# Optimization experiments

Hardware: AMD Instinct MI355X
Metric: run time of the kernel (lower is better)

The kernel has to match this reference:

```python
import jax, jax.numpy as jnp
import numpy as np

HQ, HKV, D, NE = 8, 2, 48, 384   # query heads, kv heads, head_size, n_embd
GROUP = HQ // HKV                # query heads per kv head (repeat_interleave factor)
ROPE_BASE = 10000
NEG_INF = -1e30


def rope_cache(T, head_dim):
    # matches build_rope_cache: inv_freq over even indices, angles = pos * inv_freq
    inv_freq = 1.0 / (ROPE_BASE ** (jnp.arange(0, head_dim, 2, dtype=jnp.float32) / head_dim))
    pos = jnp.arange(T, dtype=jnp.float32)
    ang = pos[:, None] * inv_freq[None, :]          # [T, D/2]
    return jnp.cos(ang), jnp.sin(ang)


def apply_rope(x, cos, sin):
    # interleaved (even/odd) rotation, re-interleaved via stack+reshape
    xe = x[..., 0::2]
    xo = x[..., 1::2]
    re = xe * cos - xo * sin
    ro = xe * sin + xo * cos
    return jnp.stack((re, ro), axis=-1).reshape(x.shape)


def setup_inputs() -> dict:
    key = jax.random.key(0)
    ks = jax.random.split(key, 6)
    B, T = 8, 2048
    s = lambda n: 1.0 / np.sqrt(n)
    return {
        "x":  jax.random.normal(ks[0], (B, T, NE), jnp.float32),
        "wq": jax.random.normal(ks[1], (NE, HQ * D), jnp.float32) * s(NE),
        "wk": jax.random.normal(ks[2], (NE, HKV * D), jnp.float32) * s(NE),
        "wv": jax.random.normal(ks[3], (NE, HKV * D), jnp.float32) * s(NE),
        "wo": jax.random.normal(ks[4], (NE, NE), jnp.float32) * s(NE),
        "bo": jnp.zeros((NE,), jnp.float32),
    }


def reference(x, wq, wk, wv, wo, bo):
    B, T, _ = x.shape
    # QKV projections (weights stored [in, out]); [B, H, T, D]
    q = (x @ wq).reshape(B, T, HQ, D).transpose(0, 2, 1, 3)
    k = (x @ wk).reshape(B, T, HKV, D).transpose(0, 2, 1, 3)
    v = (x @ wv).reshape(B, T, HKV, D).transpose(0, 2, 1, 3)

    cos, sin = rope_cache(T, D)                      # [T, D/2]
    cos = cos[None, None]                            # [1,1,T,D/2]
    sin = sin[None, None]
    q = apply_rope(q, cos, sin)
    k = apply_rope(k, cos, sin)

    # GQA: group query heads per kv head (math-identical to repeat_interleave on k/v)
    qg = q.reshape(B, HKV, GROUP, T, D)
    scale = 1.0 / np.sqrt(D)
    scores = jnp.einsum('bhgtd,bhsd->bhgts', qg, k) * scale   # [B,HKV,G,T,T]
    causal = jnp.tril(jnp.ones((T, T), dtype=bool))
    scores = jnp.where(causal, scores, NEG_INF)
    attn = jax.nn.softmax(scores, axis=-1)
    out = jnp.einsum('bhgts,bhsd->bhgtd', attn, v)            # [B,HKV,G,T,D]
    out = out.reshape(B, HQ, T, D).transpose(0, 2, 1, 3).reshape(B, T, NE)
    # output projection (eval mode: dropout is identity)
    return out @ wo + bo
```

## Files before the change

kernel.cpp:

```cpp
#include <hip/hip_runtime.h>
#include <math.h>

#define B_   8
#define T_   2048
#define NE_  384
#define HQ_  8
#define HKV_ 2
#define D_   48
#define DH_  24

typedef __attribute__((ext_vector_type(8))) short bf16x8;
typedef __attribute__((ext_vector_type(4))) short bf16x4;
typedef __attribute__((ext_vector_type(4))) float f32x4;

static __device__ __forceinline__ short f2bf(float f) {
    union { float f; unsigned u; } v; v.f = f;
    unsigned r = (v.u + 0x7fffu + ((v.u >> 16) & 1u)) >> 16;
    return (short)r;
}

static __device__ __forceinline__ float exp2_fast(float x) {
    float r;
    asm("v_exp_f32 %0, %1" : "=v"(r) : "v"(x));
    return r;
}
static __device__ __forceinline__ unsigned cvt_pk_bf16(float lo, float hi) {
    unsigned r;
    asm("v_cvt_pk_bf16_f32 %0, %1, %2" : "=v"(r) : "v"(lo), "v"(hi));
    return r;
}
static __device__ __forceinline__ float max3f(float a, float b, float c) {
    float r;
    asm("v_max3_f32 %0, %1, %2, %3" : "=v"(r) : "v"(a), "v"(b), "v"(c));
    return r;
}
static __device__ __forceinline__ void gld16(const void* g, void* l) {
    __builtin_amdgcn_global_load_lds(
        (const __attribute__((address_space(1))) unsigned int*)g,
        (__attribute__((address_space(3))) unsigned int*)l,
        16, 0, 0);
}

__global__ __launch_bounds__(256) void prep_kernel(
    const float* __restrict__ x, const float* __restrict__ wq,
    const float* __restrict__ wk, const float* __restrict__ wv,
    const float* __restrict__ wo,
    short* __restrict__ xb, short* __restrict__ wt, short* __restrict__ wot,
    float* __restrict__ ct, float* __restrict__ st)
{
    const int bid = blockIdx.x, tid = threadIdx.x;
    if (bid < 6144) {
        int i = bid * 256 + tid;
        float4 v = ((const float4*)x)[i];
        bf16x4 o = { f2bf(v.x), f2bf(v.y), f2bf(v.z), f2bf(v.w) };
        *(bf16x4*)&xb[(size_t)i * 4] = o;
    } else if (bid < 7008) {
        int e = (bid - 6144) * 256 + tid;
        int n = e / 384, k = e - n * 384;
        float s = (n < 384) ? wq[(size_t)k * 384 + n]
                : (n < 480) ? wk[(size_t)k * 96 + (n - 384)]
                            : wv[(size_t)k * 96 + (n - 480)];
        wt[e] = f2bf(s);
    } else if (bid < 7584) {
        int e = (bid - 7008) * 256 + tid;
        int n = e / 384, k = e - n * 384;
        wot[e] = f2bf(wo[(size_t)k * 384 + n]);
    } else {
        int i = (bid - 7584) * 256 + tid;
        int t = i / DH_, j = i - t * DH_;
        double inv = pow(10000.0, -(double)(2 * j) / (double)D_);
        double ang = (double)t * inv;
        ct[i] = (float)cos(ang);
        st[i] = (float)sin(ang);
    }
}

#define GP 40
__global__ __launch_bounds__(256) void qkv_gemm_kernel(
    const short* __restrict__ xb, const short* __restrict__ wt,
    const float* __restrict__ ct, const float* __restrict__ st,
    short* __restrict__ qb, short* __restrict__ kb, short* __restrict__ vtb)
{
    const int tid = threadIdx.x;
    const int n0 = blockIdx.x * 64;
    const int m0 = blockIdx.y * 128;
    __shared__ short As[128 * GP];
    __shared__ short Bs[64 * GP];
    const int lane = tid & 63, w = tid >> 6;
    const int c = lane & 15, u = lane >> 4;
    const int mo = (w & 1) * 64, no = (w >> 1) * 32;
    f32x4 acc[4][2] = {};

    for (int kt = 0; kt < 384; kt += 32) {
        __syncthreads();
#pragma unroll
        for (int p = 0; p < 2; ++p) {
            int f = tid + p * 256;
            int row = f >> 2, j = f & 3;
            bf16x8 v = *(const bf16x8*)&xb[(size_t)(m0 + row) * 384 + kt + j * 8];
            *(bf16x8*)&As[row * GP + j * 8] = v;
        }
        {
            int row = tid >> 2, j = tid & 3;
            bf16x8 v = *(const bf16x8*)&wt[(size_t)(n0 + row) * 384 + kt + j * 8];
            *(bf16x8*)&Bs[row * GP + j * 8] = v;
        }
        __syncthreads();
        bf16x8 af[4], bfr[2];
#pragma unroll
        for (int i = 0; i < 4; ++i) af[i] = *(bf16x8*)&As[(mo + 16 * i + c) * GP + 8 * u];
#pragma unroll
        for (int j = 0; j < 2; ++j) bfr[j] = *(bf16x8*)&Bs[(no + 16 * j + c) * GP + 8 * u];
#pragma unroll
        for (int i = 0; i < 4; ++i)
#pragma unroll
            for (int j = 0; j < 2; ++j)
                acc[i][j] = __builtin_amdgcn_mfma_f32_16x16x32_bf16(af[i], bfr[j], acc[i][j], 0, 0, 0);
    }

    const float qscale = 0.14433756729740643f * 1.4426950408889634f;
#pragma unroll
    for (int i = 0; i < 4; ++i) {
#pragma unroll
        for (int j = 0; j < 2; ++j) {
            int n = n0 + no + 16 * j + c;
            int mb = m0 + mo + 16 * i + 4 * u;
            int b = mb >> 11;
            int t0 = mb & 2047;
            if (n < 480) {
                int nn = (n < 384) ? n : n - 384;
                int h = nn / 48, d = nn - h * 48;
                int fi = d >> 1;
                float sgn = (d & 1) ? 1.0f : -1.0f;
                float scl = (n < 384) ? qscale : 1.0f;
                short* dst = (n < 384) ? qb : kb;
                size_t base = (n < 384)
                    ? ((size_t)(b * HQ_ + h) * T_ + t0) * 64 + d
                    : ((size_t)(b * HKV_ + h) * T_ + t0) * 64 + d;
#pragma unroll
                for (int r = 0; r < 4; ++r) {
                    float val = acc[i][j][r];
                    float part = __shfl_xor(val, 1);
                    float cs = ct[(t0 + r) * DH_ + fi], sn = st[(t0 + r) * DH_ + fi];
                    dst[base + (size_t)r * 64] = f2bf((val * cs + sgn * part * sn) * scl);
                }
            } else {
                int nn = n - 480;
                int h = nn / 48, d = nn - h * 48;
                ushort4 pk;
                pk.x = (unsigned short)f2bf(acc[i][j][0]);
                pk.y = (unsigned short)f2bf(acc[i][j][1]);
                pk.z = (unsigned short)f2bf(acc[i][j][2]);
                pk.w = (unsigned short)f2bf(acc[i][j][3]);
                *(ushort4*)&vtb[((size_t)(b * HKV_ + h) * D_ + d) * T_ + t0] = pk;
            }
        }
    }
}

__global__ __launch_bounds__(256, 2) void attn_kernel(
    const short* __restrict__ qb, const short* __restrict__ kb,
    const short* __restrict__ vtb, short* __restrict__ aob)
{
    __shared__ __align__(16) short lds_s[14336];
    const int tid = threadIdx.x;
    const int x  = blockIdx.x;
    const int hk = blockIdx.y >> 1;
    const int gp = blockIdx.y & 1;
    const int b  = blockIdx.z;
    const int lane = tid & 63;
    const int w = tid >> 6;
    const int c = lane & 15;
    const int u = lane >> 4;

    const char* kg = (const char*)kb  + (size_t)(b * HKV_ + hk) * T_ * 128;
    const char* vg = (const char*)vtb + (size_t)(b * HKV_ + hk) * D_ * T_ * 2;

    const int swz  = (lane ^ ((lane >> 3) & 7)) << 4;
    const int vrow = lane >> 3;
    const int voff = swz & 127;

    const int mk  = (c & 7) << 4;
    const int okl = (u * 16) ^ mk;
    const int okh = (64 | (u * 16)) ^ mk;

    auto stage = [&](int bsel, int jt) {
        char* dst = (char*)lds_s + bsel * 14336;
        const char* kt = kg + (size_t)jt * 8192;
        gld16(kt + (2 * w) * 1024 + swz,     dst + (2 * w) * 1024);
        gld16(kt + (2 * w + 1) * 1024 + swz, dst + (2 * w + 1) * 1024);
        if (w < 3) {
            const char* vt = vg + (size_t)jt * 128;
            gld16(vt + (size_t)(16 * w + vrow) * 4096 + voff,
                  dst + 8192 + (2 * w) * 1024);
            gld16(vt + (size_t)(16 * w + 8 + vrow) * 4096 + voff,
                  dst + 8192 + (2 * w + 1) * 1024);
        }
    };

#pragma unroll 1
    for (int ph = 0; ph < 2; ++ph) {
        const int qt = ph ? x : 31 - x;
        bf16x8 qf0[2], qf1[2];
#pragma unroll
        for (int g = 0; g < 2; ++g) {
            int h = hk * 4 + gp * 2 + g;
            const short* qp = qb + ((size_t)(b * HQ_ + h) * T_ + qt * 64 + 16 * w + c) * 64;
            qf0[g] = *(const bf16x8*)(qp + 8 * u);
            qf1[g] = *(const bf16x8*)(qp + 32 + 8 * u);
        }
        float m_s[2] = { -1e30f, -1e30f };
        float l_s[2] = { 0.f, 0.f };
        f32x4 o[2][3] = {};

        int cur = 0;
        stage(0, 0);
        __syncthreads();

#pragma unroll 1
        for (int jt = 0; jt <= qt; ++jt) {
            if (jt < qt) stage(cur ^ 1, jt + 1);

            const bool diag = (jt == qt);
            const int mtmax = diag ? (w + 1) : 4;
            const char* kbuf = (const char*)lds_s + cur * 14336;
            const char* vbuf = kbuf + 8192;

            bf16x8 klo[4], khi[4];
            bf16x4 vf[3][4];
#pragma unroll
            for (int mt = 0; mt < 4; ++mt) {
                if (mt < mtmax) {
                    klo[mt] = *(const bf16x8*)(kbuf + mt * 2048 + c * 128 + okl);
                    khi[mt] = *(const bf16x8*)(kbuf + mt * 2048 + c * 128 + okh);
                }
            }
#pragma unroll
            for (int nt = 0; nt < 3; ++nt)
#pragma unroll
                for (int k2 = 0; k2 < 4; ++k2)
                    if (k2 < mtmax)
                        vf[nt][k2] = *(const bf16x4*)(vbuf + nt * 2048 + c * 128 +
                                                      (((k2 * 32) | (u * 8)) ^ mk));

#pragma unroll
            for (int g = 0; g < 2; ++g) {
                f32x4 s[4];
                __builtin_amdgcn_s_setprio(1);
#pragma unroll
                for (int mt = 0; mt < 4; ++mt) {
                    if (mt < mtmax) {
                        f32x4 a = {0.f, 0.f, 0.f, 0.f};
                        a = __builtin_amdgcn_mfma_f32_16x16x32_bf16(klo[mt], qf0[g], a, 0, 0, 0);
                        a = __builtin_amdgcn_mfma_f32_16x16x32_bf16(khi[mt], qf1[g], a, 0, 0, 0);
                        if (diag && mt == mtmax - 1) {
#pragma unroll
                            for (int r = 0; r < 4; ++r)
                                a[r] = (4 * u + r > c) ? -1e30f : a[r];
                        }
                        s[mt] = a;
                    }
                }
                __builtin_amdgcn_s_setprio(0);

                float mloc = -1e30f;
#pragma unroll
                for (int mt = 0; mt < 4; ++mt)
                    if (mt < mtmax)
                        mloc = max3f(max3f(s[mt][0], s[mt][1], s[mt][2]), s[mt][3], mloc);
                mloc = fmaxf(mloc, __shfl_xor(mloc, 16));
                mloc = fmaxf(mloc, __shfl_xor(mloc, 32));

                if (__any(mloc > m_s[g] + 8.0f)) {
                    float mnew = fmaxf(m_s[g], mloc);
                    float alpha = exp2_fast(m_s[g] - mnew);
                    m_s[g] = mnew;
                    l_s[g] *= alpha;
                    float a0 = __shfl(alpha, 4 * u + 0);
                    float a1 = __shfl(alpha, 4 * u + 1);
                    float a2 = __shfl(alpha, 4 * u + 2);
                    float a3 = __shfl(alpha, 4 * u + 3);
#pragma unroll
                    for (int nt = 0; nt < 3; ++nt) {
                        o[g][nt][0] *= a0; o[g][nt][1] *= a1;
                        o[g][nt][2] *= a2; o[g][nt][3] *= a3;
                    }
                }

                float psum = 0.0f;
                bf16x4 pf[4];
#pragma unroll
                for (int mt = 0; mt < 4; ++mt) {
                    if (mt < mtmax) {
                        float p0 = exp2_fast(s[mt][0] - m_s[g]);
                        float p1 = exp2_fast(s[mt][1] - m_s[g]);
                        float p2 = exp2_fast(s[mt][2] - m_s[g]);
                        float p3 = exp2_fast(s[mt][3] - m_s[g]);
                        psum += (p0 + p1) + (p2 + p3);
                        union { unsigned u2[2]; bf16x4 v; } pk;
                        pk.u2[0] = cvt_pk_bf16(p0, p1);
                        pk.u2[1] = cvt_pk_bf16(p2, p3);
                        pf[mt] = pk.v;
                    }
                }
                psum += __shfl_xor(psum, 16);
                psum += __shfl_xor(psum, 32);
                l_s[g] += psum;

                __builtin_amdgcn_s_setprio(1);
#pragma unroll
                for (int k2 = 0; k2 < 4; ++k2) {
                    if (k2 < mtmax) {
#pragma unroll
                        for (int nt = 0; nt < 3; ++nt)
                            o[g][nt] = __builtin_amdgcn_mfma_f32_16x16x16bf16_1k(
                                pf[k2], vf[nt][k2], o[g][nt], 0, 0, 0);
                    }
                }
                __builtin_amdgcn_s_setprio(0);
            }

            __syncthreads();
            cur ^= 1;
        }

#pragma unroll
        for (int g = 0; g < 2; ++g) {
            int h = hk * 4 + gp * 2 + g;
            float li = 1.0f / l_s[g];
            float l0 = __shfl(li, 4 * u + 0);
            float l1 = __shfl(li, 4 * u + 1);
            float l2 = __shfl(li, 4 * u + 2);
            float l3 = __shfl(li, 4 * u + 3);
            float lr[4] = { l0, l1, l2, l3 };
#pragma unroll
            for (int nt = 0; nt < 3; ++nt)
#pragma unroll
                for (int r = 0; r < 4; ++r) {
                    int t = qt * 64 + 16 * w + 4 * u + r;
                    aob[((size_t)b * T_ + t) * NE_ + h * D_ + 16 * nt + c] =
                        f2bf(o[g][nt][r] * lr[r]);
                }
        }
    }
}

__global__ __launch_bounds__(256) void out_gemm_kernel(
    const short* __restrict__ aob, const short* __restrict__ wot,
    const float* __restrict__ bias, float* __restrict__ out)
{
    const int tid = threadIdx.x;
    const int n0 = blockIdx.x * 64;
    const int m0 = blockIdx.y * 128;
    __shared__ short As[128 * GP];
    __shared__ short Bs[64 * GP];
    const int lane = tid & 63, w = tid >> 6;
    const int c = lane & 15, u = lane >> 4;
    const int mo = (w & 1) * 64, no = (w >> 1) * 32;
    f32x4 acc[4][2] = {};

    for (int kt = 0; kt < 384; kt += 32) {
        __syncthreads();
#pragma unroll
        for (int p = 0; p < 2; ++p) {
            int f = tid + p * 256;
            int row = f >> 2, j = f & 3;
            bf16x8 v = *(const bf16x8*)&aob[(size_t)(m0 + row) * 384 + kt + j * 8];
            *(bf16x8*)&As[row * GP + j * 8] = v;
        }
        {
            int row = tid >> 2, j = tid & 3;
            bf16x8 v = *(const bf16x8*)&wot[(size_t)(n0 + row) * 384 + kt + j * 8];
            *(bf16x8*)&Bs[row * GP + j * 8] = v;
        }
        __syncthreads();
        bf16x8 af[4], bfr[2];
#pragma unroll
        for (int i = 0; i < 4; ++i) af[i] = *(bf16x8*)&As[(mo + 16 * i + c) * GP + 8 * u];
#pragma unroll
        for (int j = 0; j < 2; ++j) bfr[j] = *(bf16x8*)&Bs[(no + 16 * j + c) * GP + 8 * u];
#pragma unroll
        for (int i = 0; i < 4; ++i)
#pragma unroll
            for (int j = 0; j < 2; ++j)
                acc[i][j] = __builtin_amdgcn_mfma_f32_16x16x32_bf16(af[i], bfr[j], acc[i][j], 0, 0, 0);
    }

#pragma unroll
    for (int i = 0; i < 4; ++i) {
#pragma unroll
        for (int j = 0; j < 2; ++j) {
            int n = n0 + no + 16 * j + c;
            int mb = m0 + mo + 16 * i + 4 * u;
            float bv = bias[n];
#pragma unroll
            for (int r = 0; r < 4; ++r)
                out[(size_t)(mb + r) * 384 + n] = acc[i][j][r] + bv;
        }
    }
}

extern "C" void kernel_launch(void* const* d_in, const int* in_sizes, int n_in,
                              void* d_out, int out_size, void* d_ws, size_t ws_size,
                              hipStream_t stream) {
    const float* x  = (const float*)d_in[0];
    const float* wq = (const float*)d_in[1];
    const float* wk = (const float*)d_in[2];
    const float* wv = (const float*)d_in[3];
    const float* wo = (const float*)d_in[4];
    const float* bo = (const float*)d_in[5];
    float* out = (float*)d_out;

    float* ct  = (float*)d_ws;
    float* st  = ct + 49152;
    short* xb  = (short*)(st + 49152);
    short* wt  = xb  + (size_t)16384 * 384;
    short* wot = wt  + (size_t)576 * 384;
    short* qb  = wot + (size_t)384 * 384;
    short* kb  = qb  + (size_t)B_ * HQ_  * T_ * 64;
    short* vtb = kb  + (size_t)B_ * HKV_ * T_ * 64;
    short* aob = vtb + (size_t)B_ * HKV_ * D_ * T_;

    hipLaunchKernelGGL(prep_kernel, dim3(7776), dim3(256), 0, stream,
                       x, wq, wk, wv, wo, xb, wt, wot, ct, st);
    hipMemsetAsync(qb, 0, ((size_t)B_ * HQ_ * T_ * 64 + (size_t)B_ * HKV_ * T_ * 64) * sizeof(short), stream);
    hipLaunchKernelGGL(qkv_gemm_kernel, dim3(9, 128), dim3(256), 0, stream,
                       xb, wt, ct, st, qb, kb, vtb);
    hipLaunchKernelGGL(attn_kernel, dim3(16, 4, 8), dim3(256), 0, stream,
                       qb, kb, vtb, aob);
    hipLaunchKernelGGL(out_gemm_kernel, dim3(6, 128), dim3(256), 0, stream,
                       aob, wot, bo, out);
}
```

Measured before the change: 210.4 us.

## Double-buffer GEMMs with async global-to-LDS loads and split attention q-tile pairing

The QKV and output GEMMs now use a double-buffered, XOR-swizzled LDS layout filled by direct global-to-LDS 16-byte loads with a K step of 64. This overlaps the next tile's loads with the current MFMAs and halves the number of barriers. The attention kernel drops the pairing of two causal q-tiles per block and launches one q-tile per block over twice as many blocks, in reverse order so the longest tiles start first. This trades the built-in load balance of pairing for more parallelism and simpler control, and the GEMM LDS use rises to 48KB per block, which may reduce occupancy.

```diff
diff --git a/kernel.cpp b/kernel.cpp
--- a/kernel.cpp
+++ b/kernel.cpp
@@ -75,47 +75,60 @@
     }
 }
 
-#define GP 40
 __global__ __launch_bounds__(256) void qkv_gemm_kernel(
     const short* __restrict__ xb, const short* __restrict__ wt,
     const float* __restrict__ ct, const float* __restrict__ st,
     short* __restrict__ qb, short* __restrict__ kb, short* __restrict__ vtb)
 {
+    __shared__ __align__(16) char ldsb[49152];
     const int tid = threadIdx.x;
     const int n0 = blockIdx.x * 64;
     const int m0 = blockIdx.y * 128;
-    __shared__ short As[128 * GP];
-    __shared__ short Bs[64 * GP];
     const int lane = tid & 63, w = tid >> 6;
     const int c = lane & 15, u = lane >> 4;
     const int mo = (w & 1) * 64, no = (w >> 1) * 32;
+    const int lrow = lane >> 3;
+    const int lcol = (((lane & 7) ^ lrow) << 4);
     f32x4 acc[4][2] = {};
 
-    for (int kt = 0; kt < 384; kt += 32) {
+    auto stage = [&](int bsel, int t) {
+        char* dst = ldsb + bsel * 24576;
+        const char* Ag = (const char*)xb + (size_t)(m0 + w * 32 + lrow) * 768 + t * 128 + lcol;
+#pragma unroll
+        for (int p = 0; p < 4; ++p)
+            gld16(Ag + p * 8 * 768, dst + w * 4096 + p * 1024);
+        const char* Bg = (const char*)wt + (size_t)(n0 + w * 16 + lrow) * 768 + t * 128 + lcol;
+#pragma unroll
+        for (int p = 0; p < 2; ++p)
+            gld16(Bg + p * 8 * 768, dst + 16384 + w * 2048 + p * 1024);
+    };
+
+    stage(0, 0);
+    __syncthreads();
+    int cur = 0;
+#pragma unroll 1
+    for (int t = 0; t < 6; ++t) {
+        if (t < 5) stage(cur ^ 1, t + 1);
+        const char* Ab = ldsb + cur * 24576;
+        const char* Bb = Ab + 16384;
+#pragma unroll
+        for (int kk = 0; kk < 2; ++kk) {
+            const int off = (kk * 64 + u * 16) ^ ((c & 7) << 4);
+            bf16x8 af[4], bfr[2];
+#pragma unroll
+            for (int i = 0; i < 4; ++i)
+                af[i] = *(const bf16x8*)(Ab + (mo + 16 * i + c) * 128 + off);
+#pragma unroll
+            for (int j = 0; j < 2; ++j)
+                bfr[j] = *(const bf16x8*)(Bb + (no + 16 * j + c) * 128 + off);
+#pragma unroll
+            for (int i = 0; i < 4; ++i)
+#pragma unroll
+                for (int j = 0; j < 2; ++j)
+                    acc[i][j] = __builtin_amdgcn_mfma_f32_16x16x32_bf16(af[i], bfr[j], acc[i][j], 0, 0, 0);
+        }
         __syncthreads();
-#pragma unroll
-        for (int p = 0; p < 2; ++p) {
-            int f = tid + p * 256;
-            int row = f >> 2, j = f & 3;
-            bf16x8 v = *(const bf16x8*)&xb[(size_t)(m0 + row) * 384 + kt + j * 8];
-            *(bf16x8*)&As[row * GP + j * 8] = v;
-        }
-        {
-            int row = tid >> 2, j = tid & 3;
-            bf16x8 v = *(const bf16x8*)&wt[(size_t)(n0 + row) * 384 + kt + j * 8];
-            *(bf16x8*)&Bs[row * GP + j * 8] = v;
-        }
-        __syncthreads();
-        bf16x8 af[4], bfr[2];
-#pragma unroll
-        for (int i = 0; i < 4; ++i) af[i] = *(bf16x8*)&As[(mo + 16 * i + c) * GP + 8 * u];
-#pragma unroll
-        for (int j = 0; j < 2; ++j) bfr[j] = *(bf16x8*)&Bs[(no + 16 * j + c) * GP + 8 * u];
-#pragma unroll
-        for (int i = 0; i < 4; ++i)
-#pragma unroll
-            for (int j = 0; j < 2; ++j)
-                acc[i][j] = __builtin_amdgcn_mfma_f32_16x16x32_bf16(af[i], bfr[j], acc[i][j], 0, 0, 0);
+        cur ^= 1;
     }
 
     const float qscale = 0.14433756729740643f * 1.4426950408889634f;
@@ -164,7 +177,7 @@
 {
     __shared__ __align__(16) short lds_s[14336];
     const int tid = threadIdx.x;
-    const int x  = blockIdx.x;
+    const int qt = 31 - blockIdx.x;
     const int hk = blockIdx.y >> 1;
     const int gp = blockIdx.y & 1;
     const int b  = blockIdx.z;
@@ -198,150 +211,146 @@
         }
     };
 
+    bf16x8 qf0[2], qf1[2];
+#pragma unroll
+    for (int g = 0; g < 2; ++g) {
+        int h = hk * 4 + gp * 2 + g;
+        const short* qp = qb + ((size_t)(b * HQ_ + h) * T_ + qt * 64 + 16 * w + c) * 64;
+        qf0[g] = *(const bf16x8*)(qp + 8 * u);
+        qf1[g] = *(const bf16x8*)(qp + 32 + 8 * u);
+    }
+    float m_s[2] = { -1e30f, -1e30f };
+    float l_s[2] = { 0.f, 0.f };
+    f32x4 o[2][3] = {};
+
+    int cur = 0;
+    stage(0, 0);
+    __syncthreads();
+
 #pragma unroll 1
-    for (int ph = 0; ph < 2; ++ph) {
-        const int qt = ph ? x : 31 - x;
-        bf16x8 qf0[2], qf1[2];
+    for (int jt = 0; jt <= qt; ++jt) {
+        if (jt < qt) stage(cur ^ 1, jt + 1);
+
+        const bool diag = (jt == qt);
+        const int mtmax = diag ? (w + 1) : 4;
+        const char* kbuf = (const char*)lds_s + cur * 14336;
+        const char* vbuf = kbuf + 8192;
+
+        bf16x8 klo[4], khi[4];
+        bf16x4 vf[3][4];
+#pragma unroll
+        for (int mt = 0; mt < 4; ++mt) {
+            if (mt < mtmax) {
+                klo[mt] = *(const bf16x8*)(kbuf + mt * 2048 + c * 128 + okl);
+                khi[mt] = *(const bf16x8*)(kbuf + mt * 2048 + c * 128 + okh);
+            }
+        }
+#pragma unroll
+        for (int nt = 0; nt < 3; ++nt)
+#pragma unroll
+            for (int k2 = 0; k2 < 4; ++k2)
+                if (k2 < mtmax)
+                    vf[nt][k2] = *(const bf16x4*)(vbuf + nt * 2048 + c * 128 +
+                                                  (((k2 * 32) | (u * 8)) ^ mk));
+
 #pragma unroll
         for (int g = 0; g < 2; ++g) {
-            int h = hk * 4 + gp * 2 + g;
-            const short* qp = qb + ((size_t)(b * HQ_ + h) * T_ + qt * 64 + 16 * w + c) * 64;
-            qf0[g] = *(const bf16x8*)(qp + 8 * u);
-            qf1[g] = *(const bf16x8*)(qp + 32 + 8 * u);
-        }
-        float m_s[2] = { -1e30f, -1e30f };
-        float l_s[2] = { 0.f, 0.f };
-        f32x4 o[2][3] = {};
-
-        int cur = 0;
-        stage(0, 0);
-        __syncthreads();
-
-#pragma unroll 1
-        for (int jt = 0; jt <= qt; ++jt) {
-            if (jt < qt) stage(cur ^ 1, jt + 1);
-
-            const bool diag = (jt == qt);
-            const int mtmax = diag ? (w + 1) : 4;
-            const char* kbuf = (const char*)lds_s + cur * 14336;
-            const char* vbuf = kbuf + 8192;
-
-            bf16x8 klo[4], khi[4];
-            bf16x4 vf[3][4];
+            f32x4 s[4];
+            __builtin_amdgcn_s_setprio(1);
 #pragma unroll
             for (int mt = 0; mt < 4; ++mt) {
                 if (mt < mtmax) {
-                    klo[mt] = *(const bf16x8*)(kbuf + mt * 2048 + c * 128 + okl);
-                    khi[mt] = *(const bf16x8*)(kbuf + mt * 2048 + c * 128 + okh);
+                    f32x4 a = {0.f, 0.f, 0.f, 0.f};
+                    a = __builtin_amdgcn_mfma_f32_16x16x32_bf16(klo[mt], qf0[g], a, 0, 0, 0);
+                    a = __builtin_amdgcn_mfma_f32_16x16x32_bf16(khi[mt], qf1[g], a, 0, 0, 0);
+                    if (diag && mt == mtmax - 1) {
+#pragma unroll
+                        for (int r = 0; r < 4; ++r)
+                            a[r] = (4 * u + r > c) ? -1e30f : a[r];
+                    }
+                    s[mt] = a;
                 }
             }
-#pragma unroll
-            for (int nt = 0; nt < 3; ++nt)
-#pragma unroll
-                for (int k2 = 0; k2 < 4; ++k2)
-                    if (k2 < mtmax)
-                        vf[nt][k2] = *(const bf16x4*)(vbuf + nt * 2048 + c * 128 +
-                                                      (((k2 * 32) | (u * 8)) ^ mk));
-
-#pragma unroll
-            for (int g = 0; g < 2; ++g) {
-                f32x4 s[4];
-                __builtin_amdgcn_s_setprio(1);
-#pragma unroll
-                for (int mt = 0; mt < 4; ++mt) {
-                    if (mt < mtmax) {
-                        f32x4 a = {0.f, 0.f, 0.f, 0.f};
-                        a = __builtin_amdgcn_mfma_f32_16x16x32_bf16(klo[mt], qf0[g], a, 0, 0, 0);
-                        a = __builtin_amdgcn_mfma_f32_16x16x32_bf16(khi[mt], qf1[g], a, 0, 0, 0);
-                        if (diag && mt == mtmax - 1) {
-#pragma unroll
-                            for (int r = 0; r < 4; ++r)
-                                a[r] = (4 * u + r > c) ? -1e30f : a[r];
-                        }
-                        s[mt] = a;
-                    }
+            __builtin_amdgcn_s_setprio(0);
+
+            float mloc = -1e30f;
+#pragma unroll
+            for (int mt = 0; mt < 4; ++mt)
+                if (mt < mtmax)
+                    mloc = max3f(max3f(s[mt][0], s[mt][1], s[mt][2]), s[mt][3], mloc);
+            mloc = fmaxf(mloc, __shfl_xor(mloc, 16));
+            mloc = fmaxf(mloc, __shfl_xor(mloc, 32));
+
+            if (__any(mloc > m_s[g] + 8.0f)) {
+                float mnew = fmaxf(m_s[g], mloc);
+                float alpha = exp2_fast(m_s[g] - mnew);
+                m_s[g] = mnew;
+                l_s[g] *= alpha;
+                float a0 = __shfl(alpha, 4 * u + 0);
+                float a1 = __shfl(alpha, 4 * u + 1);
+                float a2 = __shfl(alpha, 4 * u + 2);
+                float a3 = __shfl(alpha, 4 * u + 3);
+#pragma unroll
+                for (int nt = 0; nt < 3; ++nt) {
+                    o[g][nt][0] *= a0; o[g][nt][1] *= a1;
+                    o[g][nt][2] *= a2; o[g][nt][3] *= a3;
                 }
-                __builtin_amdgcn_s_setprio(0);
-
-                float mloc = -1e30f;
-#pragma unroll
-                for (int mt = 0; mt < 4; ++mt)
-                    if (mt < mtmax)
-                        mloc = max3f(max3f(s[mt][0], s[mt][1], s[mt][2]), s[mt][3], mloc);
-                mloc = fmaxf(mloc, __shfl_xor(mloc, 16));
-                mloc = fmaxf(mloc, __shfl_xor(mloc, 32));
-
-                if (__any(mloc > m_s[g] + 8.0f)) {
-                    float mnew = fmaxf(m_s[g], mloc);
-                    float alpha = exp2_fast(m_s[g] - mnew);
-                    m_s[g] = mnew;
-                    l_s[g] *= alpha;
-                    float a0 = __shfl(alpha, 4 * u + 0);
-                    float a1 = __shfl(alpha, 4 * u + 1);
-                    float a2 = __shfl(alpha, 4 * u + 2);
-                    float a3 = __shfl(alpha, 4 * u + 3);
-#pragma unroll
-                    for (int nt = 0; nt < 3; ++nt) {
-                        o[g][nt][0] *= a0; o[g][nt][1] *= a1;
-                        o[g][nt][2] *= a2; o[g][nt][3] *= a3;
-                    }
+            }
+
+            float psum = 0.0f;
+            bf16x4 pf[4];
+#pragma unroll
+            for (int mt = 0; mt < 4; ++mt) {
+                if (mt < mtmax) {
+                    float p0 = exp2_fast(s[mt][0] - m_s[g]);
+                    float p1 = exp2_fast(s[mt][1] - m_s[g]);
+                    float p2 = exp2_fast(s[mt][2] - m_s[g]);
+                    float p3 = exp2_fast(s[mt][3] - m_s[g]);
+                    psum += (p0 + p1) + (p2 + p3);
+                    union { unsigned u2[2]; bf16x4 v; } pk;
+                    pk.u2[0] = cvt_pk_bf16(p0, p1);
+                    pk.u2[1] = cvt_pk_bf16(p2, p3);
+                    pf[mt] = pk.v;
                 }
-
-                float psum = 0.0f;
-                bf16x4 pf[4];
-#pragma unroll
-                for (int mt = 0; mt < 4; ++mt) {
-                    if (mt < mtmax) {
-                        float p0 = exp2_fast(s[mt][0] - m_s[g]);
-                        float p1 = exp2_fast(s[mt][1] - m_s[g]);
-                        float p2 = exp2_fast(s[mt][2] - m_s[g]);
-                        float p3 = exp2_fast(s[mt][3] - m_s[g]);
-                        psum += (p0 + p1) + (p2 + p3);
-                        union { unsigned u2[2]; bf16x4 v; } pk;
-                        pk.u2[0] = cvt_pk_bf16(p0, p1);
-                        pk.u2[1] = cvt_pk_bf16(p2, p3);
-                        pf[mt] = pk.v;
-                    }
+            }
+            psum += __shfl_xor(psum, 16);
+            psum += __shfl_xor(psum, 32);
+            l_s[g] += psum;
+
+            __builtin_amdgcn_s_setprio(1);
+#pragma unroll
+            for (int k2 = 0; k2 < 4; ++k2) {
+                if (k2 < mtmax) {
+#pragma unroll
+                    for (int nt = 0; nt < 3; ++nt)
+                        o[g][nt] = __builtin_amdgcn_mfma_f32_16x16x16bf16_1k(
+                            pf[k2], vf[nt][k2], o[g][nt], 0, 0, 0);
                 }
-                psum += __shfl_xor(psum, 16);
-                psum += __shfl_xor(psum, 32);
-                l_s[g] += psum;
-
-                __builtin_amdgcn_s_setprio(1);
-#pragma unroll
-                for (int k2 = 0; k2 < 4; ++k2) {
-                    if (k2 < mtmax) {
-#pragma unroll
-                        for (int nt = 0; nt < 3; ++nt)
-                            o[g][nt] = __builtin_amdgcn_mfma_f32_16x16x16bf16_1k(
-                                pf[k2], vf[nt][k2], o[g][nt], 0, 0, 0);
-                    }
-                }
-                __builtin_amdgcn_s_setprio(0);
-            }
-
-            __syncthreads();
-            cur ^= 1;
-        }
-
-#pragma unroll
-        for (int g = 0; g < 2; ++g) {
-            int h = hk * 4 + gp * 2 + g;
-            float li = 1.0f / l_s[g];
-            float l0 = __shfl(li, 4 * u + 0);
-            float l1 = __shfl(li, 4 * u + 1);
-            float l2 = __shfl(li, 4 * u + 2);
-            float l3 = __shfl(li, 4 * u + 3);
-            float lr[4] = { l0, l1, l2, l3 };
-#pragma unroll
-            for (int nt = 0; nt < 3; ++nt)
-#pragma unroll
-                for (int r = 0; r < 4; ++r) {
-                    int t = qt * 64 + 16 * w + 4 * u + r;
-                    aob[((size_t)b * T_ + t) * NE_ + h * D_ + 16 * nt + c] =
-                        f2bf(o[g][nt][r] * lr[r]);
-                }
-        }
+            }
+            __builtin_amdgcn_s_setprio(0);
+        }
+
+        __syncthreads();
+        cur ^= 1;
+    }
+
+#pragma unroll
+    for (int g = 0; g < 2; ++g) {
+        int h = hk * 4 + gp * 2 + g;
+        float li = 1.0f / l_s[g];
+        float l0 = __shfl(li, 4 * u + 0);
+        float l1 = __shfl(li, 4 * u + 1);
+        float l2 = __shfl(li, 4 * u + 2);
+        float l3 = __shfl(li, 4 * u + 3);
+        float lr[4] = { l0, l1, l2, l3 };
+#pragma unroll
+        for (int nt = 0; nt < 3; ++nt)
+#pragma unroll
+            for (int r = 0; r < 4; ++r) {
+                int t = qt * 64 + 16 * w + 4 * u + r;
+                aob[((size_t)b * T_ + t) * NE_ + h * D_ + 16 * nt + c] =
+                    f2bf(o[g][nt][r] * lr[r]);
+            }
     }
 }
 
@@ -349,41 +358,55 @@
     const short* __restrict__ aob, const short* __restrict__ wot,
     const float* __restrict__ bias, float* __restrict__ out)
 {
+    __shared__ __align__(16) char ldsb[49152];
     const int tid = threadIdx.x;
     const int n0 = blockIdx.x * 64;
     const int m0 = blockIdx.y * 128;
-    __shared__ short As[128 * GP];
-    __shared__ short Bs[64 * GP];
     const int lane = tid & 63, w = tid >> 6;
     const int c = lane & 15, u = lane >> 4;
     const int mo = (w & 1) * 64, no = (w >> 1) * 32;
+    const int lrow = lane >> 3;
+    const int lcol = (((lane & 7) ^ lrow) << 4);
     f32x4 acc[4][2] = {};
 
-    for (int kt = 0; kt < 384; kt += 32) {
+    auto stage = [&](int bsel, int t) {
+        char* dst = ldsb + bsel * 24576;
+        const char* Ag = (const char*)aob + (size_t)(m0 + w * 32 + lrow) * 768 + t * 128 + lcol;
+#pragma unroll
+        for (int p = 0; p < 4; ++p)
+            gld16(Ag + p * 8 * 768, dst + w * 4096 + p * 1024);
+        const char* Bg = (const char*)wot + (size_t)(n0 + w * 16 + lrow) * 768 + t * 128 + lcol;
+#pragma unroll
+        for (int p = 0; p < 2; ++p)
+            gld16(Bg + p * 8 * 768, dst + 16384 + w * 2048 + p * 1024);
+    };
+
+    stage(0, 0);
+    __syncthreads();
+    int cur = 0;
+#pragma unroll 1
+    for (int t = 0; t < 6; ++t) {
+        if (t < 5) stage(cur ^ 1, t + 1);
+        const char* Ab = ldsb + cur * 24576;
+        const char* Bb = Ab + 16384;
+#pragma unroll
+        for (int kk = 0; kk < 2; ++kk) {
+            const int off = (kk * 64 + u * 16) ^ ((c & 7) << 4);
+            bf16x8 af[4], bfr[2];
+#pragma unroll
+            for (int i = 0; i < 4; ++i)
+                af[i] = *(const bf16x8*)(Ab + (mo + 16 * i + c) * 128 + off);
+#pragma unroll
+            for (int j = 0; j < 2; ++j)
+                bfr[j] = *(const bf16x8*)(Bb + (no + 16 * j + c) * 128 + off);
+#pragma unroll
+            for (int i = 0; i < 4; ++i)
+#pragma unroll
+                for (int j = 0; j < 2; ++j)
+                    acc[i][j] = __builtin_amdgcn_mfma_f32_16x16x32_bf16(af[i], bfr[j], acc[i][j], 0, 0, 0);
+        }
         __syncthreads();
-#pragma unroll
-        for (int p = 0; p < 2; ++p) {
-            int f = tid + p * 256;
-            int row = f >> 2, j = f & 3;
-            bf16x8 v = *(const bf16x8*)&aob[(size_t)(m0 + row) * 384 + kt + j * 8];
-            *(bf16x8*)&As[row * GP + j * 8] = v;
-        }
-        {
-            int row = tid >> 2, j = tid & 3;
-            bf16x8 v = *(const bf16x8*)&wot[(size_t)(n0 + row) * 384 + kt + j * 8];
-            *(bf16x8*)&Bs[row * GP + j * 8] = v;
-        }
-        __syncthreads();
-        bf16x8 af[4], bfr[2];
-#pragma unroll
-        for (int i = 0; i < 4; ++i) af[i] = *(bf16x8*)&As[(mo + 16 * i + c) * GP + 8 * u];
-#pragma unroll
-        for (int j = 0; j < 2; ++j) bfr[j] = *(bf16x8*)&Bs[(no + 16 * j + c) * GP + 8 * u];
-#pragma unroll
-        for (int i = 0; i < 4; ++i)
-#pragma unroll
-            for (int j = 0; j < 2; ++j)
-                acc[i][j] = __builtin_amdgcn_mfma_f32_16x16x32_bf16(af[i], bfr[j], acc[i][j], 0, 0, 0);
+        cur ^= 1;
     }
 
 #pragma unroll
@@ -426,7 +449,7 @@
     hipMemsetAsync(qb, 0, ((size_t)B_ * HQ_ * T_ * 64 + (size_t)B_ * HKV_ * T_ * 64) * sizeof(short), stream);
     hipLaunchKernelGGL(qkv_gemm_kernel, dim3(9, 128), dim3(256), 0, stream,
                        xb, wt, ct, st, qb, kb, vtb);
-    hipLaunchKernelGGL(attn_kernel, dim3(16, 4, 8), dim3(256), 0, stream,
+    hipLaunchKernelGGL(attn_kernel, dim3(32, 4, 8), dim3(256), 0, stream,
                        qb, kb, vtb, aob);
     hipLaunchKernelGGL(out_gemm_kernel, dim3(6, 128), dim3(256), 0, stream,
                        aob, wot, bo, out);
```

After: 262.3 us. +24.6%, slower.
